# Optimization experiments

Hardware: AMD Instinct MI355X
Metric: run time of the kernel (lower is better)

Reference implementation:

```python
import jax, jax.numpy as jnp
import numpy as np

B, L, E, DK = 16, 2048, 1024, 128
MODE = "Decoder"


def setup_inputs() -> dict:
    key = jax.random.key(0)
    ks = jax.random.split(key, 6)
    x = jax.random.normal(ks[0], (B, L, E), dtype=jnp.float32)
    context = jax.random.normal(ks[1], (B, L, E), dtype=jnp.float32)
    batch_lengths = jax.random.randint(ks[2], (B,), 1, L + 1)  # valid lengths in [1, L]
    Wq = jax.random.normal(ks[3], (E, DK), dtype=jnp.float32) * 0.02
    Wk = jax.random.normal(ks[4], (E, DK), dtype=jnp.float32) * 0.02
    Wv = jax.random.normal(ks[5], (E, DK), dtype=jnp.float32) * 0.02
    return {"x": x, "context": context, "batch_lengths": batch_lengths,
            "Wq": Wq, "Wk": Wk, "Wv": Wv, "max_len": L}


def reference(x, context, batch_lengths, Wq, Wk, Wv, max_len):
    # x, context: [B, L, E]; batch_lengths: [B] ints; weights: [E, DK]
    Lq = x.shape[1]
    dk = Wq.shape[1]
    pos = jnp.arange(Lq)
    # outputMask: zero out padded time steps, broadcast over feature dim [B, L, 1]
    len_mask = (pos[None, :] < batch_lengths[:, None]).astype(x.dtype)[:, :, None]
    Q = (context @ Wq) * len_mask
    K = (context @ Wk) * len_mask
    V = (x @ Wv) * len_mask
    # energy: [B, Lq, Lk]
    energy = jnp.einsum("bqd,bkd->bqk", Q, K)
    # attnMask: -inf on padded key positions
    key_valid = pos[None, None, :] < batch_lengths[:, None, None]  # [B,1,Lk]
    if MODE == "Decoder":
        causal = pos[None, :, None] >= pos[None, None, :]  # j <= i
        key_valid = key_valid & causal
    energy = jnp.where(key_valid, energy, -jnp.inf)
    score = jax.nn.softmax(energy / jnp.sqrt(jnp.asarray(dk, x.dtype)), axis=-1)
    return jnp.einsum("bqk,bkd->bqd", score, V)
```

## Files before the change

kernel.cpp:

```cpp
#include <hip/hip_runtime.h>

#define DEV __device__ __forceinline__

typedef __attribute__((ext_vector_type(4))) float f32x4;
typedef __attribute__((ext_vector_type(4))) unsigned short u16x4;
typedef __attribute__((ext_vector_type(8))) __bf16 bf16x8;

constexpr int NB = 16, SL = 2048, EM = 1024, DKD = 128;

DEV unsigned short f2bf(float f) {
  unsigned int u = __float_as_uint(f);
  u += 0x7FFFu + ((u >> 16) & 1u);
  return (unsigned short)(u >> 16);
}

DEV f32x4 mfma16(bf16x8 a, bf16x8 b, f32x4 c) {
  return __builtin_amdgcn_mfma_f32_16x16x32_bf16(a, b, c, 0, 0, 0);
}

DEV void dma16(const void* g, void* l) {
  __builtin_amdgcn_global_load_lds(
      (const __attribute__((address_space(1))) unsigned int*)g,
      (__attribute__((address_space(3))) unsigned int*)l, 16, 0, 0);
}

DEV bf16x8 cvt8(f32x4 a, f32x4 b) {
  bf16x8 r;
  r[0] = (__bf16)a[0]; r[1] = (__bf16)a[1]; r[2] = (__bf16)a[2]; r[3] = (__bf16)a[3];
  r[4] = (__bf16)b[0]; r[5] = (__bf16)b[1]; r[6] = (__bf16)b[2]; r[7] = (__bf16)b[3];
  return r;
}

#define SBAR() __builtin_amdgcn_sched_barrier(0)

__global__ __launch_bounds__(256) void prep_w(
    const float* __restrict__ Wq, const float* __restrict__ Wk,
    const float* __restrict__ Wv, unsigned short* __restrict__ Wt,
    float* __restrict__ mvg)
{
  __shared__ unsigned short T[64 * 128];
  const int tid = threadIdx.x;
  if (blockIdx.x == 0) {
    #pragma unroll
    for (int i = 0; i < NB * DKD / 256; ++i) mvg[i * 256 + tid] = 0.f;
  }
  const int m = blockIdx.x >> 4, kc = blockIdx.x & 15;
  const float* W = (m == 0) ? Wq : ((m == 1) ? Wk : Wv);
  #pragma unroll
  for (int it = 0; it < 8; ++it) {
    int idx = it * 256 + tid;
    int kk = idx >> 5, n4 = (idx & 31) * 4;
    f32x4 w4 = *(const f32x4*)(W + (size_t)(kc * 64 + kk) * DKD + n4);
    *(u16x4*)&T[kk * 128 + n4] =
        u16x4{ f2bf(w4[0]), f2bf(w4[1]), f2bf(w4[2]), f2bf(w4[3]) };
  }
  __syncthreads();
  #pragma unroll
  for (int it = 0; it < 4; ++it) {
    int idx = it * 256 + tid;
    int p = idx & 7, n = idx >> 3;
    int c = p ^ (n & 7);
    unsigned short v[8];
    #pragma unroll
    for (int e = 0; e < 8; ++e) v[e] = T[(c * 8 + e) * 128 + n];
    size_t t = ((size_t)(m * 16 + kc) * 128 + n) * 8 + p;
    *(u16x4*)(Wt + t * 8)     = u16x4{v[0], v[1], v[2], v[3]};
    *(u16x4*)(Wt + t * 8 + 4) = u16x4{v[4], v[5], v[6], v[7]};
  }
}

__global__ __launch_bounds__(256, 2) void proj_qk(
    const float* __restrict__ ctx, const unsigned short* __restrict__ Wt,
    const int* __restrict__ lens, unsigned short* __restrict__ Qo,
    unsigned short* __restrict__ Kz)
{
  __shared__ float Als[2][64 * 64];
  const int tid = threadIdx.x;
  const int wave = tid >> 6, lane = tid & 63;
  const int quad = lane >> 4, mm = lane & 15;
  const int rb = blockIdx.x * 64;
  const int len = lens[blockIdx.x >> 5];
  if ((rb & (SL - 1)) >= len) return;

  f32x4 acc[4][4];
  #pragma unroll
  for (int i = 0; i < 4; ++i)
    #pragma unroll
    for (int j = 0; j < 4; ++j) acc[i][j] = f32x4{0.f, 0.f, 0.f, 0.f};

  const float* asrc[4];
  #pragma unroll
  for (int i = 0; i < 4; ++i) {
    const int rl_ = wave * 16 + i * 4 + (lane >> 4);
    const int cc  = (lane & 8) | ((lane & 7) ^ (rl_ & 7));
    asrc[i] = ctx + (size_t)(rb + rl_) * EM + cc * 4;
  }
  int soff[2][2];
  #pragma unroll
  for (int ks = 0; ks < 2; ++ks) {
    soff[ks][0] = (ks * 8 + ((quad * 2)     ^ (mm & 7))) * 4;
    soff[ks][1] = (ks * 8 + ((quad * 2 + 1) ^ (mm & 7))) * 4;
  }
  const unsigned short* bbase[4][2];
  #pragma unroll
  for (int lo = 0; lo < 4; ++lo)
    #pragma unroll
    for (int ks = 0; ks < 2; ++ks) {
      const int nrow = (wave * 4 + lo) * 16 + mm;
      const int pp = (ks * 4 + quad) ^ (mm & 7);
      const int cs = nrow * 8 + pp;
      bbase[lo][ks] = Wt + ((size_t)(cs >> 10) * 16384 + (cs & 1023)) * 8;
    }

  #pragma unroll
  for (int i = 0; i < 4; ++i)
    dma16(asrc[i],      (char*)Als[0] + wave * 4096 + i * 1024);
  #pragma unroll
  for (int i = 0; i < 4; ++i)
    dma16(asrc[i] + 64, (char*)Als[1] + wave * 4096 + i * 1024);
  __asm__ volatile("s_waitcnt vmcnt(4)" ::: "memory");
  __builtin_amdgcn_s_barrier();

  #pragma unroll 1
  for (int kc = 0; kc < 16; ++kc) {
    SBAR();
    bf16x8 bfr[4][2];
    #pragma unroll
    for (int lo = 0; lo < 4; ++lo)
      #pragma unroll
      for (int ks = 0; ks < 2; ++ks)
        bfr[lo][ks] = *(const bf16x8*)(bbase[lo][ks] + (size_t)kc * 8192);
    bf16x8 af[4][2];
    #pragma unroll
    for (int rt = 0; rt < 4; ++rt) {
      const float* rbase = Als[kc & 1] + (rt * 16 + mm) * 64;
      #pragma unroll
      for (int ks = 0; ks < 2; ++ks) {
        f32x4 a0 = *(const f32x4*)(rbase + soff[ks][0]);
        f32x4 a1 = *(const f32x4*)(rbase + soff[ks][1]);
        af[rt][ks] = cvt8(a0, a1);
      }
    }
    __asm__ volatile("s_waitcnt lgkmcnt(0)" ::: "memory");
    SBAR();
    __builtin_amdgcn_s_barrier();
    {
      const int kn = (kc + 2 < 16) ? (kc + 2) : 15;
      #pragma unroll
      for (int i = 0; i < 4; ++i)
        dma16(asrc[i] + kn * 64, (char*)Als[kc & 1] + wave * 4096 + i * 1024);
    }
    #pragma unroll
    for (int lo = 0; lo < 4; ++lo)
      #pragma unroll
      for (int ks = 0; ks < 2; ++ks)
        #pragma unroll
        for (int rt = 0; rt < 4; ++rt)
          acc[rt][lo] = mfma16(af[rt][ks], bfr[lo][ks], acc[rt][lo]);
    __builtin_amdgcn_s_barrier();
  }
  __asm__ volatile("s_waitcnt vmcnt(0)" ::: "memory");

  const float SCALE = 1.4426950408889634f * 0.08838834764831845f;
  #pragma unroll
  for (int rt = 0; rt < 4; ++rt)
    #pragma unroll
    for (int lo = 0; lo < 4; ++lo) {
      const int ctg = wave * 4 + lo;
      #pragma unroll
      for (int reg = 0; reg < 4; ++reg) {
        const int row = rb + rt * 16 + quad * 4 + reg;
        const int j = row & (SL - 1);
        const float val = acc[rt][lo][reg];
        if (ctg < 8) {
          const int d = ctg * 16 + mm;
          Qo[(size_t)row * DKD + d] = f2bf(val * ((j < len) ? SCALE : 0.f));
        } else {
          const int d = (ctg - 8) * 16 + mm;
          Kz[(size_t)row * DKD + (((d >> 3) ^ (j & 15)) * 8) + (d & 7)] = f2bf(val);
        }
      }
    }
}

__global__ __launch_bounds__(256, 2) void proj_v(
    const float* __restrict__ x, const unsigned short* __restrict__ Wt,
    const int* __restrict__ lens, unsigned short* __restrict__ Vz,
    float* __restrict__ mvg)
{
  __shared__ float Als[2][64 * 64];
  const int tid = threadIdx.x;
  const int wave = tid >> 6, lane = tid & 63;
  const int quad = lane >> 4, mm = lane & 15;
  const int rb = blockIdx.x * 64;
  const int bidx = blockIdx.x >> 5;
  const int len = lens[bidx];
  if ((rb & (SL - 1)) >= len) return;

  f32x4 acc[4][2];
  #pragma unroll
  for (int i = 0; i < 4; ++i) { acc[i][0] = f32x4{0.f,0.f,0.f,0.f}; acc[i][1] = f32x4{0.f,0.f,0.f,0.f}; }

  const float* asrc[4];
  #pragma unroll
  for (int i = 0; i < 4; ++i) {
    const int rl_ = wave * 16 + i * 4 + (lane >> 4);
    const int cc  = (lane & 8) | ((lane & 7) ^ (rl_ & 7));
    asrc[i] = x + (size_t)(rb + rl_) * EM + cc * 4;
  }
  int soff[2][2];
  #pragma unroll
  for (int ks = 0; ks < 2; ++ks) {
    soff[ks][0] = (ks * 8 + ((quad * 2)     ^ (mm & 7))) * 4;
    soff[ks][1] = (ks * 8 + ((quad * 2 + 1) ^ (mm & 7))) * 4;
  }
  const unsigned short* bbase[2][2];
  #pragma unroll
  for (int lo = 0; lo < 2; ++lo)
    #pragma unroll
    for (int ks = 0; ks < 2; ++ks) {
      const int nrow = (wave * 2 + lo) * 16 + mm;
      const int pp = (ks * 4 + quad) ^ (mm & 7);
      const int cs = nrow * 8 + pp;
      bbase[lo][ks] = Wt + ((size_t)2 * 16384 + cs) * 8;
    }

  #pragma unroll
  for (int i = 0; i < 4; ++i)
    dma16(asrc[i],      (char*)Als[0] + wave * 4096 + i * 1024);
  #pragma unroll
  for (int i = 0; i < 4; ++i)
    dma16(asrc[i] + 64, (char*)Als[1] + wave * 4096 + i * 1024);
  __asm__ volatile("s_waitcnt vmcnt(4)" ::: "memory");
  __builtin_amdgcn_s_barrier();

  #pragma unroll 1
  for (int kc = 0; kc < 16; ++kc) {
    SBAR();
    bf16x8 bfr[2][2];
    #pragma unroll
    for (int lo = 0; lo < 2; ++lo)
      #pragma unroll
      for (int ks = 0; ks < 2; ++ks)
        bfr[lo][ks] = *(const bf16x8*)(bbase[lo][ks] + (size_t)kc * 8192);
    bf16x8 af[4][2];
    #pragma unroll
    for (int rt = 0; rt < 4; ++rt) {
      const float* rbase = Als[kc & 1] + (rt * 16 + mm) * 64;
      #pragma unroll
      for (int ks = 0; ks < 2; ++ks) {
        f32x4 a0 = *(const f32x4*)(rbase + soff[ks][0]);
        f32x4 a1 = *(const f32x4*)(rbase + soff[ks][1]);
        af[rt][ks] = cvt8(a0, a1);
      }
    }
    __asm__ volatile("s_waitcnt lgkmcnt(0)" ::: "memory");
    SBAR();
    __builtin_amdgcn_s_barrier();
    {
      const int kn = (kc + 2 < 16) ? (kc + 2) : 15;
      #pragma unroll
      for (int i = 0; i < 4; ++i)
        dma16(asrc[i] + kn * 64, (char*)Als[kc & 1] + wave * 4096 + i * 1024);
    }
    #pragma unroll
    for (int lo = 0; lo < 2; ++lo)
      #pragma unroll
      for (int ks = 0; ks < 2; ++ks)
        #pragma unroll
        for (int rt = 0; rt < 4; ++rt)
          acc[rt][lo] = mfma16(af[rt][ks], bfr[lo][ks], acc[rt][lo]);
    __builtin_amdgcn_s_barrier();
  }
  __asm__ volatile("s_waitcnt vmcnt(0)" ::: "memory");

  #pragma unroll
  for (int rt = 0; rt < 4; ++rt)
    #pragma unroll
    for (int lo = 0; lo < 2; ++lo) {
      const int d = (wave * 2 + lo) * 16 + mm;
      const int row0 = rb + rt * 16 + quad * 4;
      const int b = row0 >> 11, j0 = row0 & (SL - 1);
      u16x4 pk = u16x4{ f2bf(acc[rt][lo][0]), f2bf(acc[rt][lo][1]),
                        f2bf(acc[rt][lo][2]), f2bf(acc[rt][lo][3]) };
      size_t off = (size_t)b * DKD * SL + (size_t)d * SL + (j0 & ~63)
                 + ((((j0 >> 3) & 7) ^ (d & 7)) * 8) + (j0 & 7);
      *(u16x4*)(Vz + off) = pk;
    }

  const int jb = rb & (SL - 1);
  #pragma unroll
  for (int lo = 0; lo < 2; ++lo) {
    const int d = (wave * 2 + lo) * 16 + mm;
    float part = 0.f;
    #pragma unroll
    for (int rt = 0; rt < 4; ++rt) {
      const int jr = jb + rt * 16 + quad * 4;
      #pragma unroll
      for (int reg = 0; reg < 4; ++reg)
        if (jr + reg < len) part += acc[rt][lo][reg];
    }
    part += __shfl_xor(part, 16);
    part += __shfl_xor(part, 32);
    if (quad == 0) atomicAdd(mvg + bidx * DKD + d, part);
  }
}

__global__ __launch_bounds__(256, 2) void attn(
    const unsigned short* __restrict__ Qw, const unsigned short* __restrict__ Kz,
    const unsigned short* __restrict__ Vz, const float* __restrict__ mvg,
    const int* __restrict__ lens, float* __restrict__ out)
{
  __shared__ unsigned short Ks[2][64 * 128];
  __shared__ unsigned short Vs[2][128 * 64];
  __shared__ unsigned short Ps[4][16 * 72];
  const int tid = threadIdx.x;
  const int wave = tid >> 6, lane = tid & 63;
  const int quad = lane >> 4, mm = lane & 15;
  const int b = blockIdx.y;
  const int qb = ((int)gridDim.x - 1 - (int)blockIdx.x) * 64;
  const int len = lens[b];

  if (qb >= len) {
    const int dd = (tid & 31) * 4;
    const int r0 = tid >> 5;
    const f32x4 m4 = *(const f32x4*)(mvg + b * DKD + dd);
    const float inv = 1.0f / (float)len;
    const f32x4 val = f32x4{ m4[0]*inv, m4[1]*inv, m4[2]*inv, m4[3]*inv };
    #pragma unroll
    for (int it = 0; it < 8; ++it) {
      const int row = qb + it * 8 + r0;
      *(f32x4*)(out + ((size_t)b * SL + row) * DKD + dd) = val;
    }
    return;
  }

  const int kend = min(qb + 64, len);
  const int nblk = (kend + 63) >> 6;
  const int irow0 = qb + wave * 16 + quad * 4;

  bf16x8 aQ[4];
  {
    const unsigned short* qbase =
        Qw + (size_t)(b * SL + qb + wave * 16 + mm) * DKD + quad * 8;
    #pragma unroll
    for (int cc = 0; cc < 4; ++cc) aQ[cc] = *(const bf16x8*)(qbase + cc * 32);
  }
  bf16x8 onesb;
  #pragma unroll
  for (int i = 0; i < 8; ++i) onesb[i] = (__bf16)1.0f;

  float mr[4];
  #pragma unroll
  for (int r = 0; r < 4; ++r) mr[r] = -__builtin_inff();
  f32x4 acc[8];
  #pragma unroll
  for (int i = 0; i < 8; ++i) acc[i] = f32x4{0.f,0.f,0.f,0.f};
  f32x4 accl = f32x4{0.f,0.f,0.f,0.f};

  #pragma unroll
  for (int it = 0; it < 4; ++it) {
    int s = it * 256 + tid;
    dma16(Kz + (size_t)(b * SL) * DKD + (size_t)s * 8,
          (char*)Ks[0] + (it * 256 + wave * 64) * 16);
  }
  #pragma unroll
  for (int it = 0; it < 4; ++it) {
    int s = it * 256 + tid;
    int d = s >> 3, p = s & 7;
    dma16(Vz + (size_t)b * DKD * SL + (size_t)d * SL + p * 8,
          (char*)Vs[0] + (it * 256 + wave * 64) * 16);
  }

  #pragma unroll 1
  for (int blk = 0; blk < nblk; ++blk) {
    const int kb = blk * 64;
    __syncthreads();
    if (blk + 1 < nblk) {
      const int kb1 = kb + 64;
      const int nb = (blk + 1) & 1;
      #pragma unroll
      for (int it = 0; it < 4; ++it) {
        int s = it * 256 + tid;
        dma16(Kz + (size_t)(b * SL + kb1) * DKD + (size_t)s * 8,
              (char*)Ks[nb] + (it * 256 + wave * 64) * 16);
      }
      #pragma unroll
      for (int it = 0; it < 4; ++it) {
        int s = it * 256 + tid;
        int d = s >> 3, p = s & 7;
        dma16(Vz + (size_t)b * DKD * SL + (size_t)d * SL + kb1 + p * 8,
              (char*)Vs[nb] + (it * 256 + wave * 64) * 16);
      }
    }
    const unsigned short* kbuf = Ks[blk & 1];
    const unsigned short* vbuf = Vs[blk & 1];

    f32x4 s4[4];
    #pragma unroll
    for (int nt = 0; nt < 4; ++nt) {
      f32x4 c = f32x4{0.f,0.f,0.f,0.f};
      const int j = nt * 16 + mm;
      #pragma unroll
      for (int cc = 0; cc < 4; ++cc) {
        const int pp = (cc * 4 + quad) ^ mm;
        bf16x8 kf = *(const bf16x8*)(kbuf + j * 128 + pp * 8);
        c = mfma16(aQ[cc], kf, c);
      }
      s4[nt] = c;
    }

    float alpha[4];
    #pragma unroll
    for (int reg = 0; reg < 4; ++reg) {
      const int jl = min(irow0 + reg + 1, len);
      float v0 = (kb + mm      < jl) ? s4[0][reg] : -__builtin_inff();
      float v1 = (kb + 16 + mm < jl) ? s4[1][reg] : -__builtin_inff();
      float v2 = (kb + 32 + mm < jl) ? s4[2][reg] : -__builtin_inff();
      float v3 = (kb + 48 + mm < jl) ? s4[3][reg] : -__builtin_inff();
      float mx = fmaxf(fmaxf(v0, v1), fmaxf(v2, v3));
      #pragma unroll
      for (int xm = 1; xm < 16; xm <<= 1) mx = fmaxf(mx, __shfl_xor(mx, xm));
      const float mn = fmaxf(mr[reg], mx);
      alpha[reg] = __builtin_amdgcn_exp2f(mr[reg] - mn);
      const float p0 = __builtin_amdgcn_exp2f(v0 - mn);
      const float p1 = __builtin_amdgcn_exp2f(v1 - mn);
      const float p2 = __builtin_amdgcn_exp2f(v2 - mn);
      const float p3 = __builtin_amdgcn_exp2f(v3 - mn);
      mr[reg] = mn;
      const int prow = quad * 4 + reg;
      Ps[wave][prow * 72 + mm]      = f2bf(p0);
      Ps[wave][prow * 72 + 16 + mm] = f2bf(p1);
      Ps[wave][prow * 72 + 32 + mm] = f2bf(p2);
      Ps[wave][prow * 72 + 48 + mm] = f2bf(p3);
    }
    #pragma unroll
    for (int nt = 0; nt < 8; ++nt) {
      f32x4 a = acc[nt];
      a[0] *= alpha[0]; a[1] *= alpha[1]; a[2] *= alpha[2]; a[3] *= alpha[3];
      acc[nt] = a;
    }
    accl[0] *= alpha[0]; accl[1] *= alpha[1];
    accl[2] *= alpha[2]; accl[3] *= alpha[3];
    __asm__ volatile("s_waitcnt lgkmcnt(0)" ::: "memory");
    bf16x8 aP[2];
    #pragma unroll
    for (int ks = 0; ks < 2; ++ks)
      aP[ks] = *(const bf16x8*)(&Ps[wave][mm * 72 + ks * 32 + quad * 8]);
    #pragma unroll
    for (int ks = 0; ks < 2; ++ks) {
      #pragma unroll
      for (int nt = 0; nt < 8; ++nt) {
        const int pp = (ks * 4 + quad) ^ (mm & 7);
        bf16x8 vf = *(const bf16x8*)(vbuf + (nt * 16 + mm) * 64 + pp * 8);
        acc[nt] = mfma16(aP[ks], vf, acc[nt]);
      }
      accl = mfma16(aP[ks], onesb, accl);
    }
  }

  #pragma unroll
  for (int reg = 0; reg < 4; ++reg) {
    const float rl = 1.0f / accl[reg];
    const size_t base = ((size_t)b * SL + irow0 + reg) * DKD + mm;
    #pragma unroll
    for (int nt = 0; nt < 8; ++nt)
      out[base + nt * 16] = acc[nt][reg] * rl;
  }
}

extern "C" void kernel_launch(void* const* d_in, const int* in_sizes, int n_in,
                              void* d_out, int out_size, void* d_ws, size_t ws_size,
                              hipStream_t stream) {
  const float* x    = (const float*)d_in[0];
  const float* ctx  = (const float*)d_in[1];
  const int*   lens = (const int*)d_in[2];
  const float* Wq   = (const float*)d_in[3];
  const float* Wk   = (const float*)d_in[4];
  const float* Wv   = (const float*)d_in[5];
  float* out = (float*)d_out;

  const size_t QKV = (size_t)NB * SL * DKD * sizeof(unsigned short);
  const size_t WTSZ = (size_t)3 * 16 * 128 * 8 * 8 * sizeof(unsigned short);
  const size_t MVSZ = (size_t)NB * DKD * sizeof(float);
  if (ws_size < 3 * QKV + WTSZ + MVSZ) return;
  unsigned short* Qws = (unsigned short*)d_ws;
  unsigned short* Kzs = (unsigned short*)((char*)d_ws + QKV);
  unsigned short* Vzs = (unsigned short*)((char*)d_ws + 2 * QKV);
  unsigned short* Wt  = (unsigned short*)((char*)d_ws + 3 * QKV);
  float*          mvg = (float*)((char*)d_ws + 3 * QKV + WTSZ);

  prep_w <<<dim3(48), 256, 0, stream>>>(Wq, Wk, Wv, Wt, mvg);
  proj_qk<<<dim3(NB * SL / 64), 256, 0, stream>>>(ctx, Wt, lens, Qws, Kzs);
  proj_v <<<dim3(NB * SL / 64), 256, 0, stream>>>(x, Wt, lens, Vzs, mvg);
  attn   <<<dim3(SL / 64, NB), 256, 0, stream>>>(Qws, Kzs, Vzs, mvg, lens, out);
}
```

Before: 346.8 us.

## Merge QK and V projections into one launch, double-buffer weight fragments, raise MFMA priority

The separate proj_qk and proj_v kernels become one launch whose blocks alternate between the QK and V paths. This removes a kernel boundary and lets both projections run concurrently. The k-loop now preloads the next weight fragments from global into a ping-pong register pair, so the B loads overlap the current MFMAs. In the attention kernel, s_setprio wraps the MFMA sections to favour matrix issue across waves. The trade-off is more register pressure and branch divergence across block types.

```diff
diff --git a/kernel.cpp b/kernel.cpp
--- a/kernel.cpp
+++ b/kernel.cpp
@@ -69,31 +69,115 @@
   }
 }
 
-__global__ __launch_bounds__(256, 2) void proj_qk(
-    const float* __restrict__ ctx, const unsigned short* __restrict__ Wt,
-    const int* __restrict__ lens, unsigned short* __restrict__ Qo,
-    unsigned short* __restrict__ Kz)
+#define QK_STEP(KC, BCUR, BNXT)                                               \
+  {                                                                           \
+    SBAR();                                                                   \
+    bf16x8 af[4][2];                                                          \
+    _Pragma("unroll")                                                         \
+    for (int rt = 0; rt < 4; ++rt) {                                          \
+      const float* rbase = Als[(KC) & 1] + (rt * 16 + mm) * 64;               \
+      _Pragma("unroll")                                                       \
+      for (int ks = 0; ks < 2; ++ks) {                                        \
+        f32x4 a0 = *(const f32x4*)(rbase + soff[ks][0]);                      \
+        f32x4 a1 = *(const f32x4*)(rbase + soff[ks][1]);                      \
+        af[rt][ks] = cvt8(a0, a1);                                            \
+      }                                                                       \
+    }                                                                         \
+    __asm__ volatile("s_waitcnt lgkmcnt(0)" ::: "memory");                    \
+    SBAR();                                                                   \
+    __builtin_amdgcn_s_barrier();            \
+    {                                                                         \
+      const int kn = ((KC) + 2 < 16) ? ((KC) + 2) : 15;                       \
+      _Pragma("unroll")                                                       \
+      for (int i = 0; i < 4; ++i)                                             \
+        dma16(asrc[i] + kn * 64,                                              \
+              (char*)Als[(KC) & 1] + wave * 4096 + i * 1024);                 \
+    }                                                                         \
+    {                                                                         \
+      const int kb1 = ((KC) + 1 < 16) ? ((KC) + 1) : 15;                      \
+      _Pragma("unroll")                                                       \
+      for (int lo = 0; lo < 4; ++lo)                                          \
+        _Pragma("unroll")                                                     \
+        for (int ks = 0; ks < 2; ++ks)                                        \
+          BNXT[lo][ks] = *(const bf16x8*)(bbase[lo][ks] + (size_t)kb1 * 8192);\
+    }                                                                         \
+    _Pragma("unroll")                                                         \
+    for (int lo = 0; lo < 4; ++lo)                                            \
+      _Pragma("unroll")                                                       \
+      for (int ks = 0; ks < 2; ++ks)                                          \
+        _Pragma("unroll")                                                     \
+        for (int rt = 0; rt < 4; ++rt)                                        \
+          acc[rt][lo] = mfma16(af[rt][ks], BCUR[lo][ks], acc[rt][lo]);        \
+    __builtin_amdgcn_s_barrier();             \
+  }
+
+#define V_STEP(KC, BCUR, BNXT)                                                \
+  {                                                                           \
+    SBAR();                                                                   \
+    bf16x8 af[4][2];                                                          \
+    _Pragma("unroll")                                                         \
+    for (int rt = 0; rt < 4; ++rt) {                                          \
+      const float* rbase = Als[(KC) & 1] + (rt * 16 + mm) * 64;               \
+      _Pragma("unroll")                                                       \
+      for (int ks = 0; ks < 2; ++ks) {                                        \
+        f32x4 a0 = *(const f32x4*)(rbase + soff[ks][0]);                      \
+        f32x4 a1 = *(const f32x4*)(rbase + soff[ks][1]);                      \
+        af[rt][ks] = cvt8(a0, a1);                                            \
+      }                                                                       \
+    }                                                                         \
+    __asm__ volatile("s_waitcnt lgkmcnt(0)" ::: "memory");                    \
+    SBAR();                                                                   \
+    __builtin_amdgcn_s_barrier();                                             \
+    {                                                                         \
+      const int kn = ((KC) + 2 < 16) ? ((KC) + 2) : 15;                       \
+      _Pragma("unroll")                                                       \
+      for (int i = 0; i < 4; ++i)                                             \
+        dma16(asrc[i] + kn * 64,                                              \
+              (char*)Als[(KC) & 1] + wave * 4096 + i * 1024);                 \
+    }                                                                         \
+    {                                                                         \
+      const int kb1 = ((KC) + 1 < 16) ? ((KC) + 1) : 15;                      \
+      _Pragma("unroll")                                                       \
+      for (int lo = 0; lo < 2; ++lo)                                          \
+        _Pragma("unroll")                                                     \
+        for (int ks = 0; ks < 2; ++ks)                                        \
+          BNXT[lo][ks] = *(const bf16x8*)(bbase[lo][ks] + (size_t)kb1 * 8192);\
+    }                                                                         \
+    _Pragma("unroll")                                                         \
+    for (int lo = 0; lo < 2; ++lo)                                            \
+      _Pragma("unroll")                                                       \
+      for (int ks = 0; ks < 2; ++ks)                                          \
+        _Pragma("unroll")                                                     \
+        for (int rt = 0; rt < 4; ++rt)                                        \
+          acc[rt][lo] = mfma16(af[rt][ks], BCUR[lo][ks], acc[rt][lo]);        \
+    __builtin_amdgcn_s_barrier();                                             \
+  }
+
+__global__ __launch_bounds__(256, 2) void proj(
+    const float* __restrict__ ctx, const float* __restrict__ x,
+    const unsigned short* __restrict__ Wt, const int* __restrict__ lens,
+    unsigned short* __restrict__ Qo, unsigned short* __restrict__ Kz,
+    unsigned short* __restrict__ Vz, float* __restrict__ mvg)
 {
   __shared__ float Als[2][64 * 64];
   const int tid = threadIdx.x;
   const int wave = tid >> 6, lane = tid & 63;
   const int quad = lane >> 4, mm = lane & 15;
-  const int rb = blockIdx.x * 64;
-  const int len = lens[blockIdx.x >> 5];
+  const int isv = blockIdx.x & 1;
+  const int bi  = (int)blockIdx.x >> 1;
+  const int rb  = bi * 64;
+  const int bidx = bi >> 5;
+  const int len = lens[bidx];
   if ((rb & (SL - 1)) >= len) return;
 
-  f32x4 acc[4][4];
-  #pragma unroll
-  for (int i = 0; i < 4; ++i)
-    #pragma unroll
-    for (int j = 0; j < 4; ++j) acc[i][j] = f32x4{0.f, 0.f, 0.f, 0.f};
+  const float* Ain = isv ? x : ctx;
 
   const float* asrc[4];
   #pragma unroll
   for (int i = 0; i < 4; ++i) {
     const int rl_ = wave * 16 + i * 4 + (lane >> 4);
     const int cc  = (lane & 8) | ((lane & 7) ^ (rl_ & 7));
-    asrc[i] = ctx + (size_t)(rb + rl_) * EM + cc * 4;
+    asrc[i] = Ain + (size_t)(rb + rl_) * EM + cc * 4;
   }
   int soff[2][2];
   #pragma unroll
@@ -101,16 +185,6 @@
     soff[ks][0] = (ks * 8 + ((quad * 2)     ^ (mm & 7))) * 4;
     soff[ks][1] = (ks * 8 + ((quad * 2 + 1) ^ (mm & 7))) * 4;
   }
-  const unsigned short* bbase[4][2];
-  #pragma unroll
-  for (int lo = 0; lo < 4; ++lo)
-    #pragma unroll
-    for (int ks = 0; ks < 2; ++ks) {
-      const int nrow = (wave * 4 + lo) * 16 + mm;
-      const int pp = (ks * 4 + quad) ^ (mm & 7);
-      const int cs = nrow * 8 + pp;
-      bbase[lo][ks] = Wt + ((size_t)(cs >> 10) * 16384 + (cs & 1023)) * 8;
-    }
 
   #pragma unroll
   for (int i = 0; i < 4; ++i)
@@ -121,188 +195,118 @@
   __asm__ volatile("s_waitcnt vmcnt(4)" ::: "memory");
   __builtin_amdgcn_s_barrier();
 
-  #pragma unroll 1
-  for (int kc = 0; kc < 16; ++kc) {
-    SBAR();
-    bf16x8 bfr[4][2];
+  if (!isv) {
+    f32x4 acc[4][4];
+    #pragma unroll
+    for (int i = 0; i < 4; ++i)
+      #pragma unroll
+      for (int j = 0; j < 4; ++j) acc[i][j] = f32x4{0.f, 0.f, 0.f, 0.f};
+
+    const unsigned short* bbase[4][2];
     #pragma unroll
     for (int lo = 0; lo < 4; ++lo)
       #pragma unroll
+      for (int ks = 0; ks < 2; ++ks) {
+        const int nrow = (wave * 4 + lo) * 16 + mm;
+        const int pp = (ks * 4 + quad) ^ (mm & 7);
+        const int cs = nrow * 8 + pp;
+        bbase[lo][ks] = Wt + ((size_t)(cs >> 10) * 16384 + (cs & 1023)) * 8;
+      }
+    bf16x8 bA[4][2], bB[4][2];
+    #pragma unroll
+    for (int lo = 0; lo < 4; ++lo)
+      #pragma unroll
       for (int ks = 0; ks < 2; ++ks)
-        bfr[lo][ks] = *(const bf16x8*)(bbase[lo][ks] + (size_t)kc * 8192);
-    bf16x8 af[4][2];
-    #pragma unroll
-    for (int rt = 0; rt < 4; ++rt) {
-      const float* rbase = Als[kc & 1] + (rt * 16 + mm) * 64;
+        bA[lo][ks] = *(const bf16x8*)(bbase[lo][ks]);
+
+    #pragma unroll 1
+    for (int t = 0; t < 8; ++t) {
+      QK_STEP(2 * t,     bA, bB)
+      QK_STEP(2 * t + 1, bB, bA)
+    }
+    __asm__ volatile("s_waitcnt vmcnt(0)" ::: "memory");
+
+    const float SCALE = 1.4426950408889634f * 0.08838834764831845f;
+    #pragma unroll
+    for (int rt = 0; rt < 4; ++rt)
+      #pragma unroll
+      for (int lo = 0; lo < 4; ++lo) {
+        const int ctg = wave * 4 + lo;
+        #pragma unroll
+        for (int reg = 0; reg < 4; ++reg) {
+          const int row = rb + rt * 16 + quad * 4 + reg;
+          const int j = row & (SL - 1);
+          const float val = acc[rt][lo][reg];
+          if (ctg < 8) {
+            const int d = ctg * 16 + mm;
+            Qo[(size_t)row * DKD + d] = f2bf(val * ((j < len) ? SCALE : 0.f));
+          } else {
+            const int d = (ctg - 8) * 16 + mm;
+            Kz[(size_t)row * DKD + (((d >> 3) ^ (j & 15)) * 8) + (d & 7)] = f2bf(val);
+          }
+        }
+      }
+  } else {
+    f32x4 acc[4][2];
+    #pragma unroll
+    for (int i = 0; i < 4; ++i) {
+      acc[i][0] = f32x4{0.f,0.f,0.f,0.f};
+      acc[i][1] = f32x4{0.f,0.f,0.f,0.f};
+    }
+    const unsigned short* bbase[2][2];
+    #pragma unroll
+    for (int lo = 0; lo < 2; ++lo)
       #pragma unroll
       for (int ks = 0; ks < 2; ++ks) {
-        f32x4 a0 = *(const f32x4*)(rbase + soff[ks][0]);
-        f32x4 a1 = *(const f32x4*)(rbase + soff[ks][1]);
-        af[rt][ks] = cvt8(a0, a1);
-      }
-    }
-    __asm__ volatile("s_waitcnt lgkmcnt(0)" ::: "memory");
-    SBAR();
-    __builtin_amdgcn_s_barrier();
-    {
-      const int kn = (kc + 2 < 16) ? (kc + 2) : 15;
-      #pragma unroll
-      for (int i = 0; i < 4; ++i)
-        dma16(asrc[i] + kn * 64, (char*)Als[kc & 1] + wave * 4096 + i * 1024);
-    }
-    #pragma unroll
-    for (int lo = 0; lo < 4; ++lo)
+        const int nrow = (wave * 2 + lo) * 16 + mm;
+        const int pp = (ks * 4 + quad) ^ (mm & 7);
+        const int cs = nrow * 8 + pp;
+        bbase[lo][ks] = Wt + ((size_t)2 * 16384 + cs) * 8;
+      }
+    bf16x8 bA[2][2], bB[2][2];
+    #pragma unroll
+    for (int lo = 0; lo < 2; ++lo)
       #pragma unroll
       for (int ks = 0; ks < 2; ++ks)
-        #pragma unroll
-        for (int rt = 0; rt < 4; ++rt)
-          acc[rt][lo] = mfma16(af[rt][ks], bfr[lo][ks], acc[rt][lo]);
-    __builtin_amdgcn_s_barrier();
-  }
-  __asm__ volatile("s_waitcnt vmcnt(0)" ::: "memory");
-
-  const float SCALE = 1.4426950408889634f * 0.08838834764831845f;
-  #pragma unroll
-  for (int rt = 0; rt < 4; ++rt)
-    #pragma unroll
-    for (int lo = 0; lo < 4; ++lo) {
-      const int ctg = wave * 4 + lo;
-      #pragma unroll
-      for (int reg = 0; reg < 4; ++reg) {
-        const int row = rb + rt * 16 + quad * 4 + reg;
-        const int j = row & (SL - 1);
-        const float val = acc[rt][lo][reg];
-        if (ctg < 8) {
-          const int d = ctg * 16 + mm;
-          Qo[(size_t)row * DKD + d] = f2bf(val * ((j < len) ? SCALE : 0.f));
-        } else {
-          const int d = (ctg - 8) * 16 + mm;
-          Kz[(size_t)row * DKD + (((d >> 3) ^ (j & 15)) * 8) + (d & 7)] = f2bf(val);
-        }
-      }
-    }
-}
-
-__global__ __launch_bounds__(256, 2) void proj_v(
-    const float* __restrict__ x, const unsigned short* __restrict__ Wt,
-    const int* __restrict__ lens, unsigned short* __restrict__ Vz,
-    float* __restrict__ mvg)
-{
-  __shared__ float Als[2][64 * 64];
-  const int tid = threadIdx.x;
-  const int wave = tid >> 6, lane = tid & 63;
-  const int quad = lane >> 4, mm = lane & 15;
-  const int rb = blockIdx.x * 64;
-  const int bidx = blockIdx.x >> 5;
-  const int len = lens[bidx];
-  if ((rb & (SL - 1)) >= len) return;
-
-  f32x4 acc[4][2];
-  #pragma unroll
-  for (int i = 0; i < 4; ++i) { acc[i][0] = f32x4{0.f,0.f,0.f,0.f}; acc[i][1] = f32x4{0.f,0.f,0.f,0.f}; }
-
-  const float* asrc[4];
-  #pragma unroll
-  for (int i = 0; i < 4; ++i) {
-    const int rl_ = wave * 16 + i * 4 + (lane >> 4);
-    const int cc  = (lane & 8) | ((lane & 7) ^ (rl_ & 7));
-    asrc[i] = x + (size_t)(rb + rl_) * EM + cc * 4;
-  }
-  int soff[2][2];
-  #pragma unroll
-  for (int ks = 0; ks < 2; ++ks) {
-    soff[ks][0] = (ks * 8 + ((quad * 2)     ^ (mm & 7))) * 4;
-    soff[ks][1] = (ks * 8 + ((quad * 2 + 1) ^ (mm & 7))) * 4;
-  }
-  const unsigned short* bbase[2][2];
-  #pragma unroll
-  for (int lo = 0; lo < 2; ++lo)
-    #pragma unroll
-    for (int ks = 0; ks < 2; ++ks) {
-      const int nrow = (wave * 2 + lo) * 16 + mm;
-      const int pp = (ks * 4 + quad) ^ (mm & 7);
-      const int cs = nrow * 8 + pp;
-      bbase[lo][ks] = Wt + ((size_t)2 * 16384 + cs) * 8;
-    }
-
-  #pragma unroll
-  for (int i = 0; i < 4; ++i)
-    dma16(asrc[i],      (char*)Als[0] + wave * 4096 + i * 1024);
-  #pragma unroll
-  for (int i = 0; i < 4; ++i)
-    dma16(asrc[i] + 64, (char*)Als[1] + wave * 4096 + i * 1024);
-  __asm__ volatile("s_waitcnt vmcnt(4)" ::: "memory");
-  __builtin_amdgcn_s_barrier();
-
-  #pragma unroll 1
-  for (int kc = 0; kc < 16; ++kc) {
-    SBAR();
-    bf16x8 bfr[2][2];
-    #pragma unroll
-    for (int lo = 0; lo < 2; ++lo)
-      #pragma unroll
-      for (int ks = 0; ks < 2; ++ks)
-        bfr[lo][ks] = *(const bf16x8*)(bbase[lo][ks] + (size_t)kc * 8192);
-    bf16x8 af[4][2];
-    #pragma unroll
-    for (int rt = 0; rt < 4; ++rt) {
-      const float* rbase = Als[kc & 1] + (rt * 16 + mm) * 64;
-      #pragma unroll
-      for (int ks = 0; ks < 2; ++ks) {
-        f32x4 a0 = *(const f32x4*)(rbase + soff[ks][0]);
-        f32x4 a1 = *(const f32x4*)(rbase + soff[ks][1]);
-        af[rt][ks] = cvt8(a0, a1);
-      }
-    }
-    __asm__ volatile("s_waitcnt lgkmcnt(0)" ::: "memory");
-    SBAR();
-    __builtin_amdgcn_s_barrier();
-    {
-      const int kn = (kc + 2 < 16) ? (kc + 2) : 15;
-      #pragma unroll
-      for (int i = 0; i < 4; ++i)
-        dma16(asrc[i] + kn * 64, (char*)Als[kc & 1] + wave * 4096 + i * 1024);
-    }
-    #pragma unroll
-    for (int lo = 0; lo < 2; ++lo)
-      #pragma unroll
-      for (int ks = 0; ks < 2; ++ks)
-        #pragma unroll
-        for (int rt = 0; rt < 4; ++rt)
-          acc[rt][lo] = mfma16(af[rt][ks], bfr[lo][ks], acc[rt][lo]);
-    __builtin_amdgcn_s_barrier();
-  }
-  __asm__ volatile("s_waitcnt vmcnt(0)" ::: "memory");
-
-  #pragma unroll
-  for (int rt = 0; rt < 4; ++rt)
+        bA[lo][ks] = *(const bf16x8*)(bbase[lo][ks]);
+
+    #pragma unroll 1
+    for (int t = 0; t < 8; ++t) {
+      V_STEP(2 * t,     bA, bB)
+      V_STEP(2 * t + 1, bB, bA)
+    }
+    __asm__ volatile("s_waitcnt vmcnt(0)" ::: "memory");
+
+    #pragma unroll
+    for (int rt = 0; rt < 4; ++rt)
+      #pragma unroll
+      for (int lo = 0; lo < 2; ++lo) {
+        const int d = (wave * 2 + lo) * 16 + mm;
+        const int row0 = rb + rt * 16 + quad * 4;
+        const int b = row0 >> 11, j0 = row0 & (SL - 1);
+        u16x4 pk = u16x4{ f2bf(acc[rt][lo][0]), f2bf(acc[rt][lo][1]),
+                          f2bf(acc[rt][lo][2]), f2bf(acc[rt][lo][3]) };
+        size_t off = (size_t)b * DKD * SL + (size_t)d * SL + (j0 & ~63)
+                   + ((((j0 >> 3) & 7) ^ (d & 7)) * 8) + (j0 & 7);
+        *(u16x4*)(Vz + off) = pk;
+      }
+
+    const int jb = rb & (SL - 1);
     #pragma unroll
     for (int lo = 0; lo < 2; ++lo) {
       const int d = (wave * 2 + lo) * 16 + mm;
-      const int row0 = rb + rt * 16 + quad * 4;
-      const int b = row0 >> 11, j0 = row0 & (SL - 1);
-      u16x4 pk = u16x4{ f2bf(acc[rt][lo][0]), f2bf(acc[rt][lo][1]),
-                        f2bf(acc[rt][lo][2]), f2bf(acc[rt][lo][3]) };
-      size_t off = (size_t)b * DKD * SL + (size_t)d * SL + (j0 & ~63)
-                 + ((((j0 >> 3) & 7) ^ (d & 7)) * 8) + (j0 & 7);
-      *(u16x4*)(Vz + off) = pk;
-    }
-
-  const int jb = rb & (SL - 1);
-  #pragma unroll
-  for (int lo = 0; lo < 2; ++lo) {
-    const int d = (wave * 2 + lo) * 16 + mm;
-    float part = 0.f;
-    #pragma unroll
-    for (int rt = 0; rt < 4; ++rt) {
-      const int jr = jb + rt * 16 + quad * 4;
-      #pragma unroll
-      for (int reg = 0; reg < 4; ++reg)
-        if (jr + reg < len) part += acc[rt][lo][reg];
-    }
-    part += __shfl_xor(part, 16);
-    part += __shfl_xor(part, 32);
-    if (quad == 0) atomicAdd(mvg + bidx * DKD + d, part);
+      float part = 0.f;
+      #pragma unroll
+      for (int rt = 0; rt < 4; ++rt) {
+        const int jr = jb + rt * 16 + quad * 4;
+        #pragma unroll
+        for (int reg = 0; reg < 4; ++reg)
+          if (jr + reg < len) part += acc[rt][lo][reg];
+      }
+      part += __shfl_xor(part, 16);
+      part += __shfl_xor(part, 32);
+      if (quad == 0) atomicAdd(mvg + bidx * DKD + d, part);
+    }
   }
 }
 
@@ -397,6 +401,7 @@
     const unsigned short* vbuf = Vs[blk & 1];
 
     f32x4 s4[4];
+    __builtin_amdgcn_s_setprio(1);
     #pragma unroll
     for (int nt = 0; nt < 4; ++nt) {
       f32x4 c = f32x4{0.f,0.f,0.f,0.f};
@@ -409,6 +414,7 @@
       }
       s4[nt] = c;
     }
+    __builtin_amdgcn_s_setprio(0);
 
     float alpha[4];
     #pragma unroll
@@ -447,6 +453,7 @@
     #pragma unroll
     for (int ks = 0; ks < 2; ++ks)
       aP[ks] = *(const bf16x8*)(&Ps[wave][mm * 72 + ks * 32 + quad * 8]);
+    __builtin_amdgcn_s_setprio(1);
     #pragma unroll
     for (int ks = 0; ks < 2; ++ks) {
       #pragma unroll
@@ -457,6 +464,7 @@
       }
       accl = mfma16(aP[ks], onesb, accl);
     }
+    __builtin_amdgcn_s_setprio(0);
   }
 
   #pragma unroll
@@ -490,8 +498,8 @@
   unsigned short* Wt  = (unsigned short*)((char*)d_ws + 3 * QKV);
   float*          mvg = (float*)((char*)d_ws + 3 * QKV + WTSZ);
 
-  prep_w <<<dim3(48), 256, 0, stream>>>(Wq, Wk, Wv, Wt, mvg);
-  proj_qk<<<dim3(NB * SL / 64), 256, 0, stream>>>(ctx, Wt, lens, Qws, Kzs);
-  proj_v <<<dim3(NB * SL / 64), 256, 0, stream>>>(x, Wt, lens, Vzs, mvg);
-  attn   <<<dim3(SL / 64, NB), 256, 0, stream>>>(Qws, Kzs, Vzs, mvg, lens, out);
-}
+  prep_w<<<dim3(48), 256, 0, stream>>>(Wq, Wk, Wv, Wt, mvg);
+  proj  <<<dim3(2 * NB * SL / 64), 256, 0, stream>>>(ctx, x, Wt, lens,
+                                                     Qws, Kzs, Vzs, mvg);
+  attn  <<<dim3(SL / 64, NB), 256, 0, stream>>>(Qws, Kzs, Vzs, mvg, lens, out);
+}
```

Measured after the change: 349.4 us. Within noise of the previous version (+0.7%).
